# Performance work log

Hardware: AMD Instinct MI355X
Metric: run time of the kernel (lower is better)

## Reference

```python
import jax, jax.numpy as jnp
import numpy as np
import math

D_MODEL = 1024
N_HEADS = 16
D_K = D_MODEL // N_HEADS
BSZ = 4
SEQ = 2048


def setup_inputs() -> dict:
    key = jax.random.key(0)
    ks = jax.random.split(key, 10)
    x = jax.random.normal(ks[0], (BSZ, SEQ, D_MODEL), dtype=jnp.float32)
    pad_mask = jnp.zeros((BSZ, 1, 1, SEQ), dtype=jnp.int32)
    s = 0.02
    Wq = jax.random.normal(ks[1], (D_MODEL, D_MODEL), jnp.float32) * s
    bq = jax.random.normal(ks[2], (D_MODEL,), jnp.float32) * s
    Wk = jax.random.normal(ks[3], (D_MODEL, D_MODEL), jnp.float32) * s
    bk = jax.random.normal(ks[4], (D_MODEL,), jnp.float32) * s
    Wv = jax.random.normal(ks[5], (D_MODEL, D_MODEL), jnp.float32) * s
    bv = jax.random.normal(ks[6], (D_MODEL,), jnp.float32) * s
    Wo = jax.random.normal(ks[7], (D_MODEL, D_MODEL), jnp.float32) * s
    bo = jax.random.normal(ks[8], (D_MODEL,), jnp.float32) * s
    return {"x": x, "pad_mask": pad_mask, "Wq": Wq, "bq": bq, "Wk": Wk,
            "bk": bk, "Wv": Wv, "bv": bv, "Wo": Wo, "bo": bo}


def reference(x, pad_mask, Wq, bq, Wk, bk, Wv, bv, Wo, bo):
    bsz, seq_len, d_model = x.shape
    h, dk = N_HEADS, D_K

    def split(W, b):
        # torch Linear: x @ W.T + b ; then [b,s,h,dk] -> [b,h,s,dk]
        y = jnp.einsum('bsd,ed->bse', x, W) + b
        return y.reshape(bsz, seq_len, h, dk).transpose(0, 2, 1, 3)

    q = split(Wq, bq)
    k = split(Wk, bk)
    v = split(Wv, bv)

    scores = jnp.einsum('bhqd,bhkd->bhqk', q, k) / math.sqrt(dk)
    causal = jnp.triu(jnp.ones((seq_len, seq_len), dtype=bool), k=1)
    scores = jnp.where(causal[None, None], -jnp.inf, scores)
    scores = jnp.where(pad_mask == 1, -jnp.inf, scores)
    attn = jax.nn.softmax(scores, axis=-1)
    attn = jnp.nan_to_num(attn, nan=0.0)
    out = jnp.einsum('bhqk,bhkd->bhqd', attn, v)
    out = out.transpose(0, 2, 1, 3).reshape(bsz, seq_len, d_model)
    # dropout is identity in eval mode
    return jnp.einsum('bsd,ed->bse', out, Wo) + bo
```

## Files before the change

kernel.cpp:

```cpp
#include <hip/hip_runtime.h>
#include <stdint.h>
#include <stddef.h>


typedef __bf16 bf16;
typedef __bf16 bf16x8 __attribute__((ext_vector_type(8)));
typedef __bf16 bf16x4 __attribute__((ext_vector_type(4)));
typedef float f32x4 __attribute__((ext_vector_type(4)));

#define DM   1024
#define NH   16
#define DK   64
#define BSZ  4
#define SEQL 2048
#define NTOK 8192
#define NEGB -3.0e38f

__device__ __forceinline__ void async16(const bf16* g, bf16* l) {
  __builtin_amdgcn_global_load_lds(
      (__attribute__((address_space(1))) void*)g,
      (__attribute__((address_space(3))) void*)l, 16, 0, 0);
}

__global__ __launch_bounds__(256) void cvt_all(
    const float* __restrict__ x,
    const float* __restrict__ w0, const float* __restrict__ w1,
    const float* __restrict__ w2, const float* __restrict__ w3,
    const int* __restrict__ pad,
    bf16* __restrict__ xd,
    bf16* __restrict__ d0, bf16* __restrict__ d1,
    bf16* __restrict__ d2, bf16* __restrict__ d3,
    float* __restrict__ padf) {
  int blk = blockIdx.x;
  if (blk >= 6144) {
    int i = (blk - 6144) * 2048 + threadIdx.x * 8;
    int4 p0 = *(const int4*)(pad + i);
    int4 p1 = *(const int4*)(pad + i + 4);
    float4 o0 = {p0.x ? NEGB : 0.f, p0.y ? NEGB : 0.f, p0.z ? NEGB : 0.f, p0.w ? NEGB : 0.f};
    float4 o1 = {p1.x ? NEGB : 0.f, p1.y ? NEGB : 0.f, p1.z ? NEGB : 0.f, p1.w ? NEGB : 0.f};
    *(float4*)(padf + i) = o0;
    *(float4*)(padf + i + 4) = o1;
    return;
  }
  const float* s; bf16* d; int i;
  if (blk < 4096) { s = x; d = xd; i = blk * 2048 + threadIdx.x * 8; }
  else {
    int m = (blk - 4096) >> 9, bi = (blk - 4096) & 511;
    switch (m) {
      case 0:  s = w0; d = d0; break;
      case 1:  s = w1; d = d1; break;
      case 2:  s = w2; d = d2; break;
      default: s = w3; d = d3; break;
    }
    i = bi * 2048 + threadIdx.x * 8;
  }
  float4 v0 = *(const float4*)(s + i);
  float4 v1 = *(const float4*)(s + i + 4);
  bf16x8 o = {(bf16)v0.x, (bf16)v0.y, (bf16)v0.z, (bf16)v0.w,
              (bf16)v1.x, (bf16)v1.y, (bf16)v1.z, (bf16)v1.w};
  *(bf16x8*)(d + i) = o;
}

template <int OUT_MODE>
__device__ __forceinline__ void gemm128(const bf16* __restrict__ A,
                                        const bf16* __restrict__ W,
                                        const float* __restrict__ bias,
                                        void* __restrict__ outp) {
  __shared__ bf16 As[128 * 32];
  __shared__ bf16 Bs[128 * 32];
  const int tid  = threadIdx.x;
  const int lane = tid & 63;
  const int wv   = tid >> 6;
  const int wm   = (wv & 1) * 64;
  const int wn   = (wv >> 1) * 64;
  const int c    = lane & 15;
  const int quad = lane >> 4;
  const int bm   = blockIdx.y * 128;
  const int bn   = blockIdx.x * 128;

  f32x4 acc[4][4] = {};

  for (int k0 = 0; k0 < DM; k0 += 32) {
    __syncthreads();
#pragma unroll
    for (int j = 0; j < 2; ++j) {
      int i = j * 256 + tid;
      async16(A + (size_t)(bm + (i >> 2)) * DM + k0 + (i & 3) * 8, As + i * 8);
      async16(W + (size_t)(bn + (i >> 2)) * DM + k0 + (i & 3) * 8, Bs + i * 8);
    }
    __syncthreads();
    bf16x8 af[4], bg[4];
#pragma unroll
    for (int mi = 0; mi < 4; ++mi)
      af[mi] = *(const bf16x8*)&As[(wm + mi * 16 + c) * 32 + quad * 8];
#pragma unroll
    for (int ni = 0; ni < 4; ++ni)
      bg[ni] = *(const bf16x8*)&Bs[(wn + ni * 16 + c) * 32 + quad * 8];
#pragma unroll
    for (int mi = 0; mi < 4; ++mi)
#pragma unroll
      for (int ni = 0; ni < 4; ++ni)
        acc[mi][ni] = __builtin_amdgcn_mfma_f32_16x16x32_bf16(af[mi], bg[ni],
                                                              acc[mi][ni], 0, 0, 0);
  }

  float bias_r[4];
#pragma unroll
  for (int ni = 0; ni < 4; ++ni) bias_r[ni] = bias[bn + wn + ni * 16 + c];

  if (OUT_MODE == 2) {
#pragma unroll
    for (int mi = 0; mi < 4; ++mi) {
      int base = bm + wm + mi * 16 + quad * 4;
      int bb = base >> 11, s0 = base & 2047;
#pragma unroll
      for (int ni = 0; ni < 4; ++ni) {
        int n_g = bn + wn + ni * 16 + c;
        int hh = n_g >> 6, dd = n_g & 63;
        bf16x4 pv = {(bf16)(acc[mi][ni][0] + bias_r[ni]),
                     (bf16)(acc[mi][ni][1] + bias_r[ni]),
                     (bf16)(acc[mi][ni][2] + bias_r[ni]),
                     (bf16)(acc[mi][ni][3] + bias_r[ni])};
        *(bf16x4*)&((bf16*)outp)[(((size_t)(bb * NH + hh)) * DK + dd) * SEQL + s0] = pv;
      }
    }
    return;
  }

#pragma unroll
  for (int mi = 0; mi < 4; ++mi) {
#pragma unroll
    for (int reg = 0; reg < 4; ++reg) {
      int m_g = bm + wm + mi * 16 + quad * 4 + reg;
#pragma unroll
      for (int ni = 0; ni < 4; ++ni) {
        int n_g = bn + wn + ni * 16 + c;
        float v = acc[mi][ni][reg] + bias_r[ni];
        if (OUT_MODE == 0) {
          int b = m_g >> 11, s = m_g & 2047;
          int h = n_g >> 6, d = n_g & 63;
          ((bf16*)outp)[(((size_t)(b * NH + h) * SEQL + s) << 6) + d] = (bf16)v;
        } else {
          ((float*)outp)[(size_t)m_g * DM + n_g] = v;
        }
      }
    }
  }
}

__global__ __launch_bounds__(256) void qkv_gemm(
    const bf16* __restrict__ X,
    const bf16* __restrict__ Wq, const bf16* __restrict__ Wk, const bf16* __restrict__ Wv,
    const float* __restrict__ bq, const float* __restrict__ bk, const float* __restrict__ bv,
    bf16* __restrict__ Q, bf16* __restrict__ K, bf16* __restrict__ Vt) {
  if (blockIdx.z == 0)      gemm128<0>(X, Wq, bq, Q);
  else if (blockIdx.z == 1) gemm128<0>(X, Wk, bk, K);
  else                      gemm128<2>(X, Wv, bv, Vt);
}

__global__ __launch_bounds__(256) void out_gemm(const bf16* __restrict__ A,
                                                const bf16* __restrict__ W,
                                                const float* __restrict__ bias,
                                                float* __restrict__ out) {
  gemm128<1>(A, W, bias, out);
}

#define PSTR 40

__global__ __launch_bounds__(256) void attn_kernel(
    const bf16* __restrict__ Q, const bf16* __restrict__ K,
    const bf16* __restrict__ Vt, const float* __restrict__ padf,
    bf16* __restrict__ O) {
  const int B = blockIdx.x;
  const int xcd = B & 7;
  const int g = B >> 3;
  const int bh = xcd + 8 * (g >> 3);
  const int t = g & 7;
  const int b = bh >> 4, h = bh & 15;
  const int tid  = threadIdx.x;
  const int lane = tid & 63;
  const int wv   = tid >> 6;
  const int c    = lane & 15;
  const int quad = lane >> 4;

  __shared__ bf16 KsS[2][32 * 64];
  __shared__ bf16 VsS[2][64 * 32];
  __shared__ bf16 Plds_all[4][32 * PSTR];
  bf16* Plds = &Plds_all[wv][0];

  const bf16* Qh  = Q  + (size_t)bh * SEQL * DK;
  const bf16* Kh  = K  + (size_t)bh * SEQL * DK;
  const bf16* Vth = Vt + (size_t)bh * DK * SEQL;
  const float* pb = padf + b * SEQL;

  const int kr = lane >> 3;
  const int kj = (lane & 7) ^ kr;
  const int vr = lane >> 2;
  const int vj = lane & 3;

  const float sc = 0.1803368801111204f;

  for (int pass = 0; pass < 2; ++pass) {
    const int qt  = pass ? 15 - t : t;
    const int R   = qt * 128 + wv * 32;
    const int nkt = (qt + 1) * 4;

    bf16x8 Qf[2][2];
#pragma unroll
    for (int qf = 0; qf < 2; ++qf)
#pragma unroll
      for (int kh = 0; kh < 2; ++kh)
        Qf[qf][kh] = *(const bf16x8*)&Qh[(size_t)(R + qf * 16 + c) * DK + kh * 32 + quad * 8];

    f32x4 Oc[2][4] = {};
    float l_s[2] = {0.f, 0.f};

    __syncthreads();
    async16(Kh + (size_t)(wv * 8 + kr) * DK + kj * 8, &KsS[0][(wv * 64 + lane) * 8]);
    async16(Vth + (size_t)(wv * 16 + vr) * SEQL + vj * 8, &VsS[0][(wv * 64 + lane) * 8]);

    for (int kt = 0; kt < nkt; ++kt) {
      const int cur = kt & 1, nxt = cur ^ 1;
      const int kb = kt * 32;
      __syncthreads();

      if (kt + 1 < nkt) {
        const int kb2 = kb + 32;
        async16(Kh + (size_t)(kb2 + wv * 8 + kr) * DK + kj * 8,
                &KsS[nxt][(wv * 64 + lane) * 8]);
        async16(Vth + (size_t)(wv * 16 + vr) * SEQL + kb2 + vj * 8,
                &VsS[nxt][(wv * 64 + lane) * 8]);
      }
      if (kb > R + 31) continue;

      float4 bc[2];
#pragma unroll
      for (int kf = 0; kf < 2; ++kf)
        bc[kf] = *(const float4*)&pb[kb + kf * 16 + quad * 4];

      bf16x8 Kf[2][2], Vf[4];
#pragma unroll
      for (int kf = 0; kf < 2; ++kf) {
        const int rloc = kf * 16 + c;
#pragma unroll
        for (int kh = 0; kh < 2; ++kh) {
          const int j = kh * 4 + quad;
          Kf[kf][kh] = *(const bf16x8*)&KsS[cur][(rloc * 8 + (j ^ (rloc & 7))) * 8];
        }
      }
#pragma unroll
      for (int df = 0; df < 4; ++df)
        Vf[df] = *(const bf16x8*)&VsS[cur][(df * 16 + c) * 32 + quad * 8];

      f32x4 st[2][2] = {};
#pragma unroll
      for (int kh = 0; kh < 2; ++kh)
#pragma unroll
        for (int kf = 0; kf < 2; ++kf)
#pragma unroll
          for (int qf = 0; qf < 2; ++qf)
            st[kf][qf] = __builtin_amdgcn_mfma_f32_16x16x32_bf16(Kf[kf][kh], Qf[qf][kh],
                                                                 st[kf][qf], 0, 0, 0);

      const bool diag = (kb + 31 > R);
#pragma unroll
      for (int qf = 0; qf < 2; ++qf) {
        float p8[8];
#pragma unroll
        for (int kf = 0; kf < 2; ++kf) {
          const float* bv4 = (const float*)&bc[kf];
#pragma unroll
          for (int r = 0; r < 4; ++r) {
            float e = __builtin_amdgcn_exp2f(__builtin_fmaf(st[kf][qf][r], sc, bv4[r]));
            if (diag && (kb + kf * 16 + quad * 4 + r > R + qf * 16 + c)) e = 0.f;
            p8[kf * 4 + r] = e;
            l_s[qf] += e;
          }
        }
        bf16x4 pk0 = {(bf16)p8[0], (bf16)p8[1], (bf16)p8[2], (bf16)p8[3]};
        bf16x4 pk1 = {(bf16)p8[4], (bf16)p8[5], (bf16)p8[6], (bf16)p8[7]};
        *(bf16x4*)&Plds[(qf * 16 + c) * PSTR + quad * 4] = pk0;
        *(bf16x4*)&Plds[(qf * 16 + c) * PSTR + 16 + quad * 4] = pk1;
      }

#pragma unroll
      for (int qf = 0; qf < 2; ++qf) {
        bf16x8 af = *(const bf16x8*)&Plds[(qf * 16 + c) * PSTR + quad * 8];
#pragma unroll
        for (int df = 0; df < 4; ++df)
          Oc[qf][df] = __builtin_amdgcn_mfma_f32_16x16x32_bf16(af, Vf[df], Oc[qf][df], 0, 0, 0);
      }
    }

#pragma unroll
    for (int qf = 0; qf < 2; ++qf) {
      float l = l_s[qf];
      l += __shfl_xor(l, 16);
      l += __shfl_xor(l, 32);
      float linv = (l > 0.f) ? 1.f / l : 0.f;
      float lr[4];
#pragma unroll
      for (int r = 0; r < 4; ++r) lr[r] = __shfl(linv, quad * 4 + r);
#pragma unroll
      for (int r = 0; r < 4; ++r) {
        size_t row = (size_t)(b * SEQL + R + qf * 16 + quad * 4 + r) * DM + h * DK;
#pragma unroll
        for (int df = 0; df < 4; ++df)
          O[row + df * 16 + c] = (bf16)(Oc[qf][df][r] * lr[r]);
      }
    }
  }
}

extern "C" void kernel_launch(void* const* d_in, const int* in_sizes, int n_in,
                              void* d_out, int out_size, void* d_ws, size_t ws_size,
                              hipStream_t stream) {
  const float* x   = (const float*)d_in[0];
  const int*   pad = (const int*)d_in[1];
  const float* Wq  = (const float*)d_in[2];
  const float* bq  = (const float*)d_in[3];
  const float* Wk  = (const float*)d_in[4];
  const float* bk  = (const float*)d_in[5];
  const float* Wv  = (const float*)d_in[6];
  const float* bv  = (const float*)d_in[7];
  const float* Wo  = (const float*)d_in[8];
  const float* bo  = (const float*)d_in[9];
  float* out = (float*)d_out;

  const size_t SZ_X = (size_t)NTOK * DM * 2;
  const size_t SZ_W = (size_t)DM * DM * 2;
  char* ws = (char*)d_ws;
  bf16* Xb  = (bf16*)ws;  ws += SZ_X;
  bf16* Wqb = (bf16*)ws;  ws += SZ_W;
  bf16* Wkb = (bf16*)ws;  ws += SZ_W;
  bf16* Wvb = (bf16*)ws;  ws += SZ_W;
  bf16* Wob = (bf16*)ws;  ws += SZ_W;
  bf16* Qb  = (bf16*)ws;  ws += SZ_X;
  bf16* Kb  = (bf16*)ws;  ws += SZ_X;
  bf16* Vtb = (bf16*)ws;  ws += SZ_X;
  bf16* Ob  = (bf16*)ws;  ws += SZ_X;
  float* padfb = (float*)ws; ws += (size_t)NTOK * 4;

  cvt_all<<<6148, 256, 0, stream>>>(x, Wq, Wk, Wv, Wo, pad,
                                    Xb, Wqb, Wkb, Wvb, Wob, padfb);
  qkv_gemm<<<dim3(8, 64, 3), 256, 0, stream>>>(Xb, Wqb, Wkb, Wvb, bq, bk, bv, Qb, Kb, Vtb);
  attn_kernel<<<512, 256, 0, stream>>>(Qb, Kb, Vtb, padfb, Ob);
  out_gemm<<<dim3(8, 64), 256, 0, stream>>>(Ob, Wob, bo, out);
}
```

Baseline: 274.8 us.

## Halve attention query tile to 16 rows per wave and stage V-transpose stores through LDS

The attention kernel now gives each wave 16 query rows instead of 32 and launches twice as many blocks, with causal tile pairing over 32 tiles. This is meant to raise parallelism and cut register pressure. The cost is that K/V tiles are loaded twice as often per head. Separately, the V-transposed epilogue of the QKV GEMM stages results in shared memory so global stores become contiguous 16-byte writes along the sequence dimension.

Result: slower. 294.0 us (+7.0%).

```diff
diff --git a/kernel.cpp b/kernel.cpp
--- a/kernel.cpp
+++ b/kernel.cpp
@@ -108,21 +108,29 @@
 #pragma unroll
   for (int ni = 0; ni < 4; ++ni) bias_r[ni] = bias[bn + wn + ni * 16 + c];
 
-  if (OUT_MODE == 2) {
-#pragma unroll
-    for (int mi = 0; mi < 4; ++mi) {
-      int base = bm + wm + mi * 16 + quad * 4;
-      int bb = base >> 11, s0 = base & 2047;
+  if constexpr (OUT_MODE == 2) {
+    __shared__ bf16 Vtr[4][64 * 72];
+    bf16* vt = &Vtr[wv][0];
+#pragma unroll
+    for (int mi = 0; mi < 4; ++mi)
 #pragma unroll
       for (int ni = 0; ni < 4; ++ni) {
-        int n_g = bn + wn + ni * 16 + c;
-        int hh = n_g >> 6, dd = n_g & 63;
         bf16x4 pv = {(bf16)(acc[mi][ni][0] + bias_r[ni]),
                      (bf16)(acc[mi][ni][1] + bias_r[ni]),
                      (bf16)(acc[mi][ni][2] + bias_r[ni]),
                      (bf16)(acc[mi][ni][3] + bias_r[ni])};
-        *(bf16x4*)&((bf16*)outp)[(((size_t)(bb * NH + hh)) * DK + dd) * SEQL + s0] = pv;
-      }
+        *(bf16x4*)&vt[(ni * 16 + c) * 72 + mi * 16 + quad * 4] = pv;
+      }
+    const int base = bm + wm;
+    const int bb = base >> 11, s0 = base & 2047;
+    const int rl = lane >> 3, cl = lane & 7;
+#pragma unroll
+    for (int it = 0; it < 8; ++it) {
+      int d_row = it * 8 + rl;
+      bf16x8 v = *(const bf16x8*)&vt[d_row * 72 + cl * 8];
+      int n_g = bn + wn + d_row;
+      int hh = n_g >> 6, dd = n_g & 63;
+      *(bf16x8*)&((bf16*)outp)[(((size_t)(bb * NH + hh)) * DK + dd) * SEQL + s0 + cl * 8] = v;
     }
     return;
   }
@@ -174,8 +182,8 @@
   const int B = blockIdx.x;
   const int xcd = B & 7;
   const int g = B >> 3;
-  const int bh = xcd + 8 * (g >> 3);
-  const int t = g & 7;
+  const int bh = xcd + 8 * (g >> 4);
+  const int t = g & 15;
   const int b = bh >> 4, h = bh & 15;
   const int tid  = threadIdx.x;
   const int lane = tid & 63;
@@ -185,7 +193,7 @@
 
   __shared__ bf16 KsS[2][32 * 64];
   __shared__ bf16 VsS[2][64 * 32];
-  __shared__ bf16 Plds_all[4][32 * PSTR];
+  __shared__ bf16 Plds_all[4][16 * PSTR];
   bf16* Plds = &Plds_all[wv][0];
 
   const bf16* Qh  = Q  + (size_t)bh * SEQL * DK;
@@ -201,19 +209,17 @@
   const float sc = 0.1803368801111204f;
 
   for (int pass = 0; pass < 2; ++pass) {
-    const int qt  = pass ? 15 - t : t;
-    const int R   = qt * 128 + wv * 32;
-    const int nkt = (qt + 1) * 4;
-
-    bf16x8 Qf[2][2];
-#pragma unroll
-    for (int qf = 0; qf < 2; ++qf)
-#pragma unroll
-      for (int kh = 0; kh < 2; ++kh)
-        Qf[qf][kh] = *(const bf16x8*)&Qh[(size_t)(R + qf * 16 + c) * DK + kh * 32 + quad * 8];
-
-    f32x4 Oc[2][4] = {};
-    float l_s[2] = {0.f, 0.f};
+    const int qt  = pass ? 31 - t : t;
+    const int R   = qt * 64 + wv * 16;
+    const int nkt = qt * 2 + 2;
+
+    bf16x8 Qf[2];
+#pragma unroll
+    for (int kh = 0; kh < 2; ++kh)
+      Qf[kh] = *(const bf16x8*)&Qh[(size_t)(R + c) * DK + kh * 32 + quad * 8];
+
+    f32x4 Oc[4] = {};
+    float l_s = 0.f;
 
     __syncthreads();
     async16(Kh + (size_t)(wv * 8 + kr) * DK + kj * 8, &KsS[0][(wv * 64 + lane) * 8]);
@@ -231,7 +237,7 @@
         async16(Vth + (size_t)(wv * 16 + vr) * SEQL + kb2 + vj * 8,
                 &VsS[nxt][(wv * 64 + lane) * 8]);
       }
-      if (kb > R + 31) continue;
+      if (kb > R + 15) continue;
 
       float4 bc[2];
 #pragma unroll
@@ -252,62 +258,51 @@
       for (int df = 0; df < 4; ++df)
         Vf[df] = *(const bf16x8*)&VsS[cur][(df * 16 + c) * 32 + quad * 8];
 
-      f32x4 st[2][2] = {};
+      f32x4 st[2] = {};
 #pragma unroll
       for (int kh = 0; kh < 2; ++kh)
 #pragma unroll
         for (int kf = 0; kf < 2; ++kf)
-#pragma unroll
-          for (int qf = 0; qf < 2; ++qf)
-            st[kf][qf] = __builtin_amdgcn_mfma_f32_16x16x32_bf16(Kf[kf][kh], Qf[qf][kh],
-                                                                 st[kf][qf], 0, 0, 0);
+          st[kf] = __builtin_amdgcn_mfma_f32_16x16x32_bf16(Kf[kf][kh], Qf[kh],
+                                                           st[kf], 0, 0, 0);
 
       const bool diag = (kb + 31 > R);
-#pragma unroll
-      for (int qf = 0; qf < 2; ++qf) {
-        float p8[8];
-#pragma unroll
-        for (int kf = 0; kf < 2; ++kf) {
-          const float* bv4 = (const float*)&bc[kf];
-#pragma unroll
-          for (int r = 0; r < 4; ++r) {
-            float e = __builtin_amdgcn_exp2f(__builtin_fmaf(st[kf][qf][r], sc, bv4[r]));
-            if (diag && (kb + kf * 16 + quad * 4 + r > R + qf * 16 + c)) e = 0.f;
-            p8[kf * 4 + r] = e;
-            l_s[qf] += e;
-          }
+      float p8[8];
+#pragma unroll
+      for (int kf = 0; kf < 2; ++kf) {
+        const float* bv4 = (const float*)&bc[kf];
+#pragma unroll
+        for (int r = 0; r < 4; ++r) {
+          float e = __builtin_amdgcn_exp2f(__builtin_fmaf(st[kf][r], sc, bv4[r]));
+          if (diag && (kb + kf * 16 + quad * 4 + r > R + c)) e = 0.f;
+          p8[kf * 4 + r] = e;
+          l_s += e;
         }
-        bf16x4 pk0 = {(bf16)p8[0], (bf16)p8[1], (bf16)p8[2], (bf16)p8[3]};
-        bf16x4 pk1 = {(bf16)p8[4], (bf16)p8[5], (bf16)p8[6], (bf16)p8[7]};
-        *(bf16x4*)&Plds[(qf * 16 + c) * PSTR + quad * 4] = pk0;
-        *(bf16x4*)&Plds[(qf * 16 + c) * PSTR + 16 + quad * 4] = pk1;
-      }
-
-#pragma unroll
-      for (int qf = 0; qf < 2; ++qf) {
-        bf16x8 af = *(const bf16x8*)&Plds[(qf * 16 + c) * PSTR + quad * 8];
-#pragma unroll
-        for (int df = 0; df < 4; ++df)
-          Oc[qf][df] = __builtin_amdgcn_mfma_f32_16x16x32_bf16(af, Vf[df], Oc[qf][df], 0, 0, 0);
-      }
-    }
-
-#pragma unroll
-    for (int qf = 0; qf < 2; ++qf) {
-      float l = l_s[qf];
-      l += __shfl_xor(l, 16);
-      l += __shfl_xor(l, 32);
-      float linv = (l > 0.f) ? 1.f / l : 0.f;
-      float lr[4];
-#pragma unroll
-      for (int r = 0; r < 4; ++r) lr[r] = __shfl(linv, quad * 4 + r);
-#pragma unroll
-      for (int r = 0; r < 4; ++r) {
-        size_t row = (size_t)(b * SEQL + R + qf * 16 + quad * 4 + r) * DM + h * DK;
-#pragma unroll
-        for (int df = 0; df < 4; ++df)
-          O[row + df * 16 + c] = (bf16)(Oc[qf][df][r] * lr[r]);
-      }
+      }
+      bf16x4 pk0 = {(bf16)p8[0], (bf16)p8[1], (bf16)p8[2], (bf16)p8[3]};
+      bf16x4 pk1 = {(bf16)p8[4], (bf16)p8[5], (bf16)p8[6], (bf16)p8[7]};
+      *(bf16x4*)&Plds[c * PSTR + quad * 4] = pk0;
+      *(bf16x4*)&Plds[c * PSTR + 16 + quad * 4] = pk1;
+
+      bf16x8 af = *(const bf16x8*)&Plds[c * PSTR + quad * 8];
+#pragma unroll
+      for (int df = 0; df < 4; ++df)
+        Oc[df] = __builtin_amdgcn_mfma_f32_16x16x32_bf16(af, Vf[df], Oc[df], 0, 0, 0);
+    }
+
+    float l = l_s;
+    l += __shfl_xor(l, 16);
+    l += __shfl_xor(l, 32);
+    float linv = (l > 0.f) ? 1.f / l : 0.f;
+    float lr[4];
+#pragma unroll
+    for (int r = 0; r < 4; ++r) lr[r] = __shfl(linv, quad * 4 + r);
+#pragma unroll
+    for (int r = 0; r < 4; ++r) {
+      size_t row = (size_t)(b * SEQL + R + quad * 4 + r) * DM + h * DK;
+#pragma unroll
+      for (int df = 0; df < 4; ++df)
+        O[row + df * 16 + c] = (bf16)(Oc[df][r] * lr[r]);
     }
   }
 }
@@ -344,6 +339,6 @@
   cvt_all<<<6148, 256, 0, stream>>>(x, Wq, Wk, Wv, Wo, pad,
                                     Xb, Wqb, Wkb, Wvb, Wob, padfb);
   qkv_gemm<<<dim3(8, 64, 3), 256, 0, stream>>>(Xb, Wqb, Wkb, Wvb, bq, bk, bv, Qb, Kb, Vtb);
-  attn_kernel<<<512, 256, 0, stream>>>(Qb, Kb, Vtb, padfb, Ob);
+  attn_kernel<<<1024, 256, 0, stream>>>(Qb, Kb, Vtb, padfb, Ob);
   out_gemm<<<dim3(8, 64), 256, 0, stream>>>(Ob, Wob, bo, out);
 }
```
